# Optimization experiments

Hardware: AMD Instinct MI355X
Metric: run time of the kernel (lower is better)

The kernel has to match this reference:

```python
import jax, jax.numpy as jnp
import numpy as np

NEG_SLOPE = 0.2  # PyG GATConv default negative_slope


def gat_layer(x, edge_index, W, att_src, att_dst, bias):
    """GATConv with self-loops, concat heads. x:[N,F_in], W:[F_in,H*C]."""
    N = x.shape[0]
    H, C = att_src.shape
    loop = jnp.arange(N, dtype=edge_index.dtype)
    src = jnp.concatenate([edge_index[0], loop])  # [E+N]
    dst = jnp.concatenate([edge_index[1], loop])
    h = (x @ W).reshape(N, H, C)                  # [N,H,C]
    a_src = jnp.einsum('nhc,hc->nh', h, att_src)  # [N,H]
    a_dst = jnp.einsum('nhc,hc->nh', h, att_dst)
    e = a_src[src] + a_dst[dst]                   # [E+N,H]
    e = jnp.where(e > 0, e, NEG_SLOPE * e)        # leaky_relu
    # numerically-stable segment softmax over incoming edges of each dst node
    m = jax.ops.segment_max(e, dst, num_segments=N)           # [N,H]
    ex = jnp.exp(e - m[dst])
    denom = jax.ops.segment_sum(ex, dst, num_segments=N)      # [N,H]
    alpha = ex / (denom[dst] + 1e-16)                          # [E+N,H]
    out = jax.ops.segment_sum(h[src] * alpha[:, :, None], dst, num_segments=N)
    return out.reshape(N, H * C) + bias


def setup_inputs() -> dict:
    key = jax.random.key(0)
    ks = jax.random.split(key, 16)
    N, E, F_IN, HID, H, NCLS = 50000, 800000, 128, 64, 4, 40
    HC = H * HID
    s = 0.1
    return {
        'x': jax.random.normal(ks[0], (N, F_IN), jnp.float32),
        'edge_index': jax.random.randint(ks[1], (2, E), 0, N, jnp.int32),
        'W1': jax.random.normal(ks[2], (F_IN, HC), jnp.float32) * s,
        'att_src1': jax.random.normal(ks[3], (H, HID), jnp.float32) * s,
        'att_dst1': jax.random.normal(ks[4], (H, HID), jnp.float32) * s,
        'b1': jnp.zeros((HC,), jnp.float32),
        'W2': jax.random.normal(ks[5], (HC, HC), jnp.float32) * s,
        'att_src2': jax.random.normal(ks[6], (H, HID), jnp.float32) * s,
        'att_dst2': jax.random.normal(ks[7], (H, HID), jnp.float32) * s,
        'b2': jnp.zeros((HC,), jnp.float32),
        'fcW1': jax.random.normal(ks[8], (HC, HID), jnp.float32) * s,
        'fcb1': jnp.zeros((HID,), jnp.float32),
        'fcW2': jax.random.normal(ks[9], (HID, NCLS), jnp.float32) * s,
        'fcb2': jnp.zeros((NCLS,), jnp.float32),
    }


def reference(x, edge_index, W1, att_src1, att_dst1, b1,
              W2, att_src2, att_dst2, b2, fcW1, fcb1, fcW2, fcb2):
    h = gat_layer(x, edge_index, W1, att_src1, att_dst1, b1)
    h = jax.nn.elu(h)
    h = gat_layer(h, edge_index, W2, att_src2, att_dst2, b2)
    h = jax.nn.elu(h)
    h = jnp.maximum(h @ fcW1 + fcb1, 0.0)  # ReLU; dropout is identity in eval
    return h @ fcW2 + fcb2                 # [N, num_classes]
```

## Files before the change

kernel.cpp:

```cpp
#include <hip/hip_runtime.h>

typedef __attribute__((ext_vector_type(8))) _Float16 fp16x8;
typedef __attribute__((ext_vector_type(4))) float f32x4;
typedef unsigned int u32;

__device__ __forceinline__ float lrelu(float x) { return x > 0.f ? x : 0.2f * x; }
__device__ __forceinline__ float elu(float x) { return x > 0.f ? x : __expf(x) - 1.f; }

__device__ __forceinline__ void gl2lds16(const void* g, void* l) {
    __builtin_amdgcn_global_load_lds((const __attribute__((address_space(1))) u32*)g,
                                     (__attribute__((address_space(3))) u32*)l, 16, 0, 0);
}

__device__ __forceinline__ void t16t_body(const float* __restrict__ W, _Float16* __restrict__ T,
                                          int N, int Nreal, int t) {
    int lane = t & 63, rem = t >> 6;
    int kk = rem & 1; rem >>= 1;
    int ncg = N / 16;
    int cg = rem % ncg, kc = rem / ncg;
    int k = kc * 64 + kk * 32 + (lane >> 4) * 8;
    int n = cg * 16 + (lane & 15);
    fp16x8 o;
#pragma unroll
    for (int j = 0; j < 8; ++j)
        o[j] = (n < Nreal) ? (_Float16)W[(size_t)(k + j) * Nreal + n] : (_Float16)0.f;
    *(fp16x8*)(T + (size_t)t * 8) = o;
}

__global__ __launch_bounds__(256) void k_prep(const float* __restrict__ W1, _Float16* __restrict__ W1T,
                                              const float* __restrict__ W2, _Float16* __restrict__ W2T,
                                              const float* __restrict__ fcW1, _Float16* __restrict__ fWT,
                                              const float* __restrict__ fcW2, _Float16* __restrict__ f2T,
                                              const int* __restrict__ dst, int* __restrict__ cnt) {
    int b = blockIdx.x, tid = threadIdx.x;
    if (b < 16)      t16t_body(W1, W1T, 256, 256, b * 256 + tid);
    else if (b < 48) t16t_body(W2, W2T, 256, 256, (b - 16) * 256 + tid);
    else if (b < 56) t16t_body(fcW1, fWT, 64, 64, (b - 48) * 256 + tid);
    else if (b < 58) t16t_body(fcW2, f2T, 64, 40, (b - 56) * 256 + tid);
    else             atomicAdd(&cnt[dst[(b - 58) * 256 + tid]], 1);
}

__global__ __launch_bounds__(256) void k_scan_a(const int* __restrict__ cnt, int* __restrict__ s,
                                                int* __restrict__ partial, int N) {
    __shared__ int sh[256];
    int t = threadIdx.x, gid = blockIdx.x * 256 + t;
    sh[t] = gid < N ? cnt[gid] : 0;
    __syncthreads();
    for (int off = 1; off < 256; off <<= 1) {
        int add = (t >= off) ? sh[t - off] : 0;
        __syncthreads();
        sh[t] += add;
        __syncthreads();
    }
    if (gid < N) s[gid] = sh[t];
    if (t == 255) partial[blockIdx.x] = sh[255];
}
__global__ __launch_bounds__(256) void k_scan_bc(const int* __restrict__ s, const int* __restrict__ partial,
                                                 const int* __restrict__ cnt, int* __restrict__ row_ptr,
                                                 int* __restrict__ cursor, int* __restrict__ bcur, int N) {
    __shared__ int red[256];
    int t = threadIdx.x, bid = blockIdx.x;
    int a = 0;
    for (int i = t; i < bid; i += 256) a += partial[i];
    red[t] = a;
    __syncthreads();
    for (int off = 128; off; off >>= 1) {
        if (t < off) red[t] += red[t + off];
        __syncthreads();
    }
    int base = red[0];
    int gid = bid * 256 + t;
    if (gid >= N) return;
    int val = s[gid] + base;
    row_ptr[gid + 1] = val;
    int excl = val - cnt[gid];
    cursor[gid] = excl;
    if ((gid & 511) == 0) bcur[gid >> 9] = excl;
    if (gid == 0) row_ptr[0] = 0;
}

__global__ __launch_bounds__(256) void k_bin(const int* __restrict__ src, const int* __restrict__ dst,
                                             int* __restrict__ bcur, int2* __restrict__ pairbuf, int E) {
    __shared__ int cnt[128], gbase[128], excl[128], cur2[128], sh[128];
    __shared__ int saddr[1024];
    __shared__ int2 spair[1024];
    const int tid = threadIdx.x;
    const int eb = blockIdx.x * 1024;
    if (tid < 128) { cnt[tid] = 0; cur2[tid] = 0; }
    __syncthreads();
    int s_[4], d_[4];
#pragma unroll
    for (int j = 0; j < 4; ++j) {
        int e = eb + j * 256 + tid;
        if (e < E) {
            s_[j] = src[e]; d_[j] = dst[e];
            atomicAdd(&cnt[d_[j] >> 9], 1);
        } else d_[j] = -1;
    }
    __syncthreads();
    if (tid < 128) sh[tid] = cnt[tid];
    __syncthreads();
    for (int off = 1; off < 128; off <<= 1) {
        int add = 0;
        if (tid < 128 && tid >= off) add = sh[tid - off];
        __syncthreads();
        if (tid < 128) sh[tid] += add;
        __syncthreads();
    }
    if (tid < 128) {
        excl[tid] = sh[tid] - cnt[tid];
        if (cnt[tid] > 0) gbase[tid] = atomicAdd(&bcur[tid], cnt[tid]);
    }
    __syncthreads();
#pragma unroll
    for (int j = 0; j < 4; ++j) {
        if (d_[j] >= 0) {
            int b = d_[j] >> 9;
            int r = atomicAdd(&cur2[b], 1);
            int slot = excl[b] + r;
            spair[slot] = make_int2(s_[j], d_[j]);
            saddr[slot] = gbase[b] + r;
        }
    }
    __syncthreads();
    int tot = min(1024, E - eb);
#pragma unroll
    for (int j = 0; j < 4; ++j) {
        int slot = j * 256 + tid;
        if (slot < tot) pairbuf[saddr[slot]] = spair[slot];
    }
}

template<int KV, int NW, int ATT, int AFP32>
__device__ __forceinline__ void gemm_body(int bid,
              const _Float16* __restrict__ Ah, const float* __restrict__ Af,
              const _Float16* __restrict__ BT, _Float16* __restrict__ Chi,
              const float* __restrict__ att_s, const float* __restrict__ att_d,
              float* __restrict__ a_src, float* __restrict__ a_dst,
              int M, int Nc) {
    constexpr int NCG = NW / 16;
    constexpr int CHUNK = NW * 64;
    constexpr int FPW = (CHUNK / 512) / 8;
    __shared__ _Float16 Bs[CHUNK];
    const int m0 = bid * 128;
    const int tid = threadIdx.x;
    const int lane = tid & 63, wv = tid >> 6;
    const int r16 = lane & 15, quad = lane >> 4;
    const int arow = min(m0 + wv * 16 + r16, M - 1);

    f32x4 acc[NCG];
#pragma unroll
    for (int cg = 0; cg < NCG; ++cg) acc[cg] = (f32x4){0, 0, 0, 0};

    constexpr int NCH = KV / 64;
#pragma unroll
    for (int kc = 0; kc < NCH; ++kc) {
        if (kc) __syncthreads();
#pragma unroll
        for (int f = 0; f < FPW; ++f) {
            int fr = wv * FPW + f;
            gl2lds16(BT + (size_t)kc * CHUNK + fr * 512 + lane * 8, &Bs[fr * 512]);
        }
        fp16x8 ar[2];
        if (AFP32) {
            const float* Ap = Af + (size_t)arow * KV + kc * 64 + quad * 8;
#pragma unroll
            for (int kk = 0; kk < 2; ++kk) {
                float4 u0 = *(const float4*)(Ap + kk * 32);
                float4 u1 = *(const float4*)(Ap + kk * 32 + 4);
                fp16x8 h8;
                h8[0] = (_Float16)u0.x; h8[1] = (_Float16)u0.y;
                h8[2] = (_Float16)u0.z; h8[3] = (_Float16)u0.w;
                h8[4] = (_Float16)u1.x; h8[5] = (_Float16)u1.y;
                h8[6] = (_Float16)u1.z; h8[7] = (_Float16)u1.w;
                ar[kk] = h8;
            }
        } else {
            const _Float16* Ahp = Ah + (size_t)arow * KV + kc * 64 + quad * 8;
#pragma unroll
            for (int kk = 0; kk < 2; ++kk) ar[kk] = *(const fp16x8*)(Ahp + kk * 32);
        }
        __syncthreads();
#pragma unroll
        for (int kk = 0; kk < 2; ++kk) {
#pragma unroll
            for (int cg = 0; cg < NCG; ++cg) {
                fp16x8 bh = *(const fp16x8*)(&Bs[(cg * 2 + kk) * 512 + lane * 8]);
                acc[cg] = __builtin_amdgcn_mfma_f32_16x16x32_f16(ar[kk], bh, acc[cg], 0, 0, 0);
            }
        }
    }

    const int rbase = m0 + wv * 16 + quad * 4;

    if (ATT) {
#pragma unroll
        for (int hq = 0; hq < 4; ++hq) {
            float as[4], ad[4];
#pragma unroll
            for (int cg = 0; cg < 4; ++cg) {
                as[cg] = att_s[hq * 64 + cg * 16 + r16];
                ad[cg] = att_d[hq * 64 + cg * 16 + r16];
            }
#pragma unroll
            for (int i = 0; i < 4; ++i) {
                float ps = acc[hq * 4 + 0][i] * as[0] + acc[hq * 4 + 1][i] * as[1]
                         + acc[hq * 4 + 2][i] * as[2] + acc[hq * 4 + 3][i] * as[3];
                float pd = acc[hq * 4 + 0][i] * ad[0] + acc[hq * 4 + 1][i] * ad[1]
                         + acc[hq * 4 + 2][i] * ad[2] + acc[hq * 4 + 3][i] * ad[3];
#pragma unroll
                for (int d = 1; d < 16; d <<= 1) {
                    ps += __shfl_xor(ps, d);
                    pd += __shfl_xor(pd, d);
                }
                int r = rbase + i;
                if (r16 == 0 && r < M) {
                    a_src[(size_t)r * 4 + hq] = ps;
                    a_dst[(size_t)r * 4 + hq] = pd;
                }
            }
        }
    }

#pragma unroll
    for (int cg = 0; cg < NCG; ++cg) {
        int c = cg * 16 + r16;
        if (c >= Nc) continue;
#pragma unroll
        for (int i = 0; i < 4; ++i) {
            int r = rbase + i;
            if (r < M) Chi[(size_t)r * Nc + c] = (_Float16)acc[cg][i];
        }
    }
}

__global__ __launch_bounds__(512, 4)
void k_work1(const float* __restrict__ x, const _Float16* __restrict__ W1T,
             _Float16* __restrict__ h,
             const float* __restrict__ att_s, const float* __restrict__ att_d,
             float* __restrict__ a_src, float* __restrict__ a_dst,
             const int2* __restrict__ pairbuf,
             int* __restrict__ cursor, int* __restrict__ csr,
             int M, int E, int RB) {
    if ((int)blockIdx.x >= RB) {
        int base = (blockIdx.x - RB) * 2048;
#pragma unroll
        for (int j = 0; j < 4; ++j) {
            int i = base + j * 512 + threadIdx.x;
            if (i < E) {
                int2 p = pairbuf[i];
                int pos = atomicAdd(&cursor[p.y], 1);
                csr[pos] = p.x;
            }
        }
        return;
    }
    gemm_body<128, 256, 1, 1>(blockIdx.x, nullptr, x, W1T, h, att_s, att_d, a_src, a_dst, M, 256);
}

#define AG2_LDA 264
__global__ __launch_bounds__(512, 4) void k_ag2(
        const _Float16* __restrict__ h, const float* __restrict__ a_src,
        const float* __restrict__ a_dst, const int* __restrict__ row_ptr,
        const int* __restrict__ csr, const float* __restrict__ bias,
        const _Float16* __restrict__ BT,
        const float* __restrict__ att_s, const float* __restrict__ att_d,
        float* __restrict__ a_src2, float* __restrict__ a_dst2,
        _Float16* __restrict__ h2, int N) {
    __shared__ _Float16 A[16 * AG2_LDA];
    __shared__ float psp[8][16], pdp[8][16];
    const int tid = threadIdx.x;
    const int n0 = blockIdx.x * 16;

    {
        int r = tid >> 5;
        int n = min(n0 + r, N - 1);
        int cl = tid & 31;
        int hd = cl >> 3;
        int beg = row_ptr[n], end = row_ptr[n + 1];
        float adh = a_dst[(size_t)4 * n + hd];
        const _Float16* hb = h + (size_t)cl * 8;

        float ws = __expf(lrelu(a_src[(size_t)4 * n + hd] + adh));
        fp16x8 sv = *(const fp16x8*)(hb + (size_t)n * 256);
        float acc[8];
#pragma unroll
        for (int j = 0; j < 8; ++j) acc[j] = ws * (float)sv[j];
        float dn = ws;

        int e = beg;
        for (; e + 4 <= end; e += 4) {
            int s0 = csr[e], s1 = csr[e + 1], s2 = csr[e + 2], s3 = csr[e + 3];
            float z0 = a_src[(size_t)4 * s0 + hd], z1 = a_src[(size_t)4 * s1 + hd];
            float z2 = a_src[(size_t)4 * s2 + hd], z3 = a_src[(size_t)4 * s3 + hd];
            fp16x8 v0 = *(const fp16x8*)(hb + (size_t)s0 * 256);
            fp16x8 v1 = *(const fp16x8*)(hb + (size_t)s1 * 256);
            fp16x8 v2 = *(const fp16x8*)(hb + (size_t)s2 * 256);
            fp16x8 v3 = *(const fp16x8*)(hb + (size_t)s3 * 256);
            float w0 = __expf(lrelu(z0 + adh)), w1 = __expf(lrelu(z1 + adh));
            float w2 = __expf(lrelu(z2 + adh)), w3 = __expf(lrelu(z3 + adh));
            dn += (w0 + w1) + (w2 + w3);
#pragma unroll
            for (int j = 0; j < 8; ++j)
                acc[j] += w0 * (float)v0[j] + w1 * (float)v1[j]
                        + w2 * (float)v2[j] + w3 * (float)v3[j];
        }
        for (; e + 2 <= end; e += 2) {
            int s0 = csr[e], s1 = csr[e + 1];
            float z0 = a_src[(size_t)4 * s0 + hd], z1 = a_src[(size_t)4 * s1 + hd];
            fp16x8 v0 = *(const fp16x8*)(hb + (size_t)s0 * 256);
            fp16x8 v1 = *(const fp16x8*)(hb + (size_t)s1 * 256);
            float w0 = __expf(lrelu(z0 + adh)), w1 = __expf(lrelu(z1 + adh));
            dn += w0 + w1;
#pragma unroll
            for (int j = 0; j < 8; ++j)
                acc[j] += w0 * (float)v0[j] + w1 * (float)v1[j];
        }
        if (e < end) {
            int s0 = csr[e];
            float w0 = __expf(lrelu(a_src[(size_t)4 * s0 + hd] + adh));
            fp16x8 v0 = *(const fp16x8*)(hb + (size_t)s0 * 256);
            dn += w0;
#pragma unroll
            for (int j = 0; j < 8; ++j) acc[j] += w0 * (float)v0[j];
        }

        float inv = 1.f / (dn + 1e-16f);
        float4 b0 = *(const float4*)(bias + cl * 8);
        float4 b1v = *(const float4*)(bias + cl * 8 + 4);
        fp16x8 hi;
        hi[0] = (_Float16)elu(acc[0] * inv + b0.x);
        hi[1] = (_Float16)elu(acc[1] * inv + b0.y);
        hi[2] = (_Float16)elu(acc[2] * inv + b0.z);
        hi[3] = (_Float16)elu(acc[3] * inv + b0.w);
        hi[4] = (_Float16)elu(acc[4] * inv + b1v.x);
        hi[5] = (_Float16)elu(acc[5] * inv + b1v.y);
        hi[6] = (_Float16)elu(acc[6] * inv + b1v.z);
        hi[7] = (_Float16)elu(acc[7] * inv + b1v.w);
        *(fp16x8*)(&A[r * AG2_LDA + cl * 8]) = hi;
    }
    __syncthreads();

    const int lane = tid & 63, wv = tid >> 6;
    const int r16 = lane & 15, quad = lane >> 4;
    f32x4 acc2[2];
    acc2[0] = (f32x4){0, 0, 0, 0};
    acc2[1] = (f32x4){0, 0, 0, 0};
#pragma unroll
    for (int kc = 0; kc < 4; ++kc) {
        fp16x8 ar[2];
#pragma unroll
        for (int kk = 0; kk < 2; ++kk)
            ar[kk] = *(const fp16x8*)(&A[r16 * AG2_LDA + kc * 64 + kk * 32 + quad * 8]);
#pragma unroll
        for (int kk = 0; kk < 2; ++kk) {
#pragma unroll
            for (int j = 0; j < 2; ++j) {
                int cg = wv * 2 + j;
                fp16x8 bh = *(const fp16x8*)(BT + ((size_t)(kc * 16 + cg) * 2 + kk) * 512 + lane * 8);
                acc2[j] = __builtin_amdgcn_mfma_f32_16x16x32_f16(ar[kk], bh, acc2[j], 0, 0, 0);
            }
        }
    }
    {
        float as[2], ad[2];
#pragma unroll
        for (int j = 0; j < 2; ++j) {
            int c = (wv * 2 + j) * 16 + r16;
            as[j] = att_s[c];
            ad[j] = att_d[c];
        }
#pragma unroll
        for (int i = 0; i < 4; ++i) {
            float ps = acc2[0][i] * as[0] + acc2[1][i] * as[1];
            float pd = acc2[0][i] * ad[0] + acc2[1][i] * ad[1];
#pragma unroll
            for (int d = 1; d < 16; d <<= 1) {
                ps += __shfl_xor(ps, d);
                pd += __shfl_xor(pd, d);
            }
            if (r16 == 0) {
                psp[wv][quad * 4 + i] = ps;
                pdp[wv][quad * 4 + i] = pd;
            }
        }
    }
#pragma unroll
    for (int j = 0; j < 2; ++j) {
        int c = (wv * 2 + j) * 16 + r16;
#pragma unroll
        for (int i = 0; i < 4; ++i) {
            int rr = n0 + quad * 4 + i;
            if (rr < N) h2[(size_t)rr * 256 + c] = (_Float16)acc2[j][i];
        }
    }
    __syncthreads();
    if (tid < 64) {
        int row = tid >> 2, hq = tid & 3;
        int rr = n0 + row;
        if (rr < N) {
            a_src2[(size_t)rr * 4 + hq] = psp[2 * hq][row] + psp[2 * hq + 1][row];
            a_dst2[(size_t)rr * 4 + hq] = pdp[2 * hq][row] + pdp[2 * hq + 1][row];
        }
    }
}

__global__ __launch_bounds__(512, 4) void k_agfc(
        const _Float16* __restrict__ h, const float* __restrict__ a_src,
        const float* __restrict__ a_dst, const int* __restrict__ row_ptr,
        const int* __restrict__ csr, const float* __restrict__ bias,
        const _Float16* __restrict__ BT1, const _Float16* __restrict__ BT2,
        const float* __restrict__ fcb1, const float* __restrict__ fcb2,
        float* __restrict__ out, int N) {
    __shared__ _Float16 A[16 * AG2_LDA];
    __shared__ _Float16 T[16 * 72];
    const int tid = threadIdx.x;
    const int n0 = blockIdx.x * 16;

    {
        int r = tid >> 5;
        int n = min(n0 + r, N - 1);
        int cl = tid & 31;
        int hd = cl >> 3;
        int beg = row_ptr[n], end = row_ptr[n + 1];
        float adh = a_dst[(size_t)4 * n + hd];
        const _Float16* hb = h + (size_t)cl * 8;

        float ws = __expf(lrelu(a_src[(size_t)4 * n + hd] + adh));
        fp16x8 sv = *(const fp16x8*)(hb + (size_t)n * 256);
        float acc[8];
#pragma unroll
        for (int j = 0; j < 8; ++j) acc[j] = ws * (float)sv[j];
        float dn = ws;

        int e = beg;
        for (; e + 4 <= end; e += 4) {
            int s0 = csr[e], s1 = csr[e + 1], s2 = csr[e + 2], s3 = csr[e + 3];
            float z0 = a_src[(size_t)4 * s0 + hd], z1 = a_src[(size_t)4 * s1 + hd];
            float z2 = a_src[(size_t)4 * s2 + hd], z3 = a_src[(size_t)4 * s3 + hd];
            fp16x8 v0 = *(const fp16x8*)(hb + (size_t)s0 * 256);
            fp16x8 v1 = *(const fp16x8*)(hb + (size_t)s1 * 256);
            fp16x8 v2 = *(const fp16x8*)(hb + (size_t)s2 * 256);
            fp16x8 v3 = *(const fp16x8*)(hb + (size_t)s3 * 256);
            float w0 = __expf(lrelu(z0 + adh)), w1 = __expf(lrelu(z1 + adh));
            float w2 = __expf(lrelu(z2 + adh)), w3 = __expf(lrelu(z3 + adh));
            dn += (w0 + w1) + (w2 + w3);
#pragma unroll
            for (int j = 0; j < 8; ++j)
                acc[j] += w0 * (float)v0[j] + w1 * (float)v1[j]
                        + w2 * (float)v2[j] + w3 * (float)v3[j];
        }
        for (; e + 2 <= end; e += 2) {
            int s0 = csr[e], s1 = csr[e + 1];
            float z0 = a_src[(size_t)4 * s0 + hd], z1 = a_src[(size_t)4 * s1 + hd];
            fp16x8 v0 = *(const fp16x8*)(hb + (size_t)s0 * 256);
            fp16x8 v1 = *(const fp16x8*)(hb + (size_t)s1 * 256);
            float w0 = __expf(lrelu(z0 + adh)), w1 = __expf(lrelu(z1 + adh));
            dn += w0 + w1;
#pragma unroll
            for (int j = 0; j < 8; ++j)
                acc[j] += w0 * (float)v0[j] + w1 * (float)v1[j];
        }
        if (e < end) {
            int s0 = csr[e];
            float w0 = __expf(lrelu(a_src[(size_t)4 * s0 + hd] + adh));
            fp16x8 v0 = *(const fp16x8*)(hb + (size_t)s0 * 256);
            dn += w0;
#pragma unroll
            for (int j = 0; j < 8; ++j) acc[j] += w0 * (float)v0[j];
        }

        float inv = 1.f / (dn + 1e-16f);
        float4 b0 = *(const float4*)(bias + cl * 8);
        float4 b1v = *(const float4*)(bias + cl * 8 + 4);
        fp16x8 hi;
        hi[0] = (_Float16)elu(acc[0] * inv + b0.x);
        hi[1] = (_Float16)elu(acc[1] * inv + b0.y);
        hi[2] = (_Float16)elu(acc[2] * inv + b0.z);
        hi[3] = (_Float16)elu(acc[3] * inv + b0.w);
        hi[4] = (_Float16)elu(acc[4] * inv + b1v.x);
        hi[5] = (_Float16)elu(acc[5] * inv + b1v.y);
        hi[6] = (_Float16)elu(acc[6] * inv + b1v.z);
        hi[7] = (_Float16)elu(acc[7] * inv + b1v.w);
        *(fp16x8*)(&A[(tid >> 5) * AG2_LDA + cl * 8]) = hi;
    }
    __syncthreads();

    const int lane = tid & 63, wv = tid >> 6;
    const int r16 = lane & 15, quad = lane >> 4;
    if (wv < 4) {
        f32x4 acc1 = (f32x4){0, 0, 0, 0};
#pragma unroll
        for (int kc = 0; kc < 4; ++kc) {
            fp16x8 ar[2];
#pragma unroll
            for (int kk = 0; kk < 2; ++kk)
                ar[kk] = *(const fp16x8*)(&A[r16 * AG2_LDA + kc * 64 + kk * 32 + quad * 8]);
#pragma unroll
            for (int kk = 0; kk < 2; ++kk) {
                fp16x8 bh = *(const fp16x8*)(BT1 + ((size_t)(kc * 4 + wv) * 2 + kk) * 512 + lane * 8);
                acc1 = __builtin_amdgcn_mfma_f32_16x16x32_f16(ar[kk], bh, acc1, 0, 0, 0);
            }
        }
        int c = wv * 16 + r16;
        float badd = fcb1[c];
#pragma unroll
        for (int i = 0; i < 4; ++i)
            T[(quad * 4 + i) * 72 + c] = (_Float16)fmaxf(acc1[i] + badd, 0.f);
    }
    __syncthreads();

    if (wv < 3) {
        fp16x8 a2[2];
#pragma unroll
        for (int kk = 0; kk < 2; ++kk)
            a2[kk] = *(const fp16x8*)(&T[r16 * 72 + kk * 32 + quad * 8]);
        f32x4 acc2 = (f32x4){0, 0, 0, 0};
#pragma unroll
        for (int kk = 0; kk < 2; ++kk) {
            fp16x8 bh = *(const fp16x8*)(BT2 + ((size_t)wv * 2 + kk) * 512 + lane * 8);
            acc2 = __builtin_amdgcn_mfma_f32_16x16x32_f16(a2[kk], bh, acc2, 0, 0, 0);
        }
        int c = wv * 16 + r16;
        if (c < 40) {
            float badd = fcb2[c];
#pragma unroll
            for (int i = 0; i < 4; ++i) {
                int rr = n0 + quad * 4 + i;
                if (rr < N) out[(size_t)rr * 40 + c] = acc2[i] + badd;
            }
        }
    }
}

extern "C" void kernel_launch(void* const* d_in, const int* in_sizes, int n_in,
                              void* d_out, int out_size, void* d_ws, size_t ws_size,
                              hipStream_t stream) {
    const int N = 50000, E = 800000, F_IN = 128, HC = 256, HID = 64, NCLS = 40;
    const float* x    = (const float*)d_in[0];
    const int*   ei   = (const int*)d_in[1];
    const float* W1   = (const float*)d_in[2];
    const float* as1  = (const float*)d_in[3];
    const float* ad1  = (const float*)d_in[4];
    const float* b1   = (const float*)d_in[5];
    const float* W2   = (const float*)d_in[6];
    const float* as2  = (const float*)d_in[7];
    const float* ad2  = (const float*)d_in[8];
    const float* b2   = (const float*)d_in[9];
    const float* fcW1 = (const float*)d_in[10];
    const float* fcb1 = (const float*)d_in[11];
    const float* fcW2 = (const float*)d_in[12];
    const float* fcb2 = (const float*)d_in[13];
    float* out = (float*)d_out;

    char* wp = (char*)d_ws;
    auto alloc = [&](size_t b) { char* p = wp; wp += (b + 255) & ~(size_t)255; return p; };
    _Float16* h     = (_Float16*)alloc((size_t)N * HC * 2);
    _Float16* ohi   = (_Float16*)alloc((size_t)N * HC * 2);
    float*  asrc  = (float*)alloc((size_t)N * 4 * 4);
    float*  adst  = (float*)alloc((size_t)N * 4 * 4);
    float*  asrc2 = (float*)alloc((size_t)N * 4 * 4);
    float*  adst2 = (float*)alloc((size_t)N * 4 * 4);
    _Float16* W1T   = (_Float16*)alloc((size_t)F_IN * HC * 2);
    _Float16* W2T   = (_Float16*)alloc((size_t)HC * HC * 2);
    _Float16* fWT   = (_Float16*)alloc((size_t)HC * HID * 2);
    _Float16* f2T   = (_Float16*)alloc((size_t)HID * HID * 2);
    int* cnt     = (int*)alloc((size_t)N * 4);
    int* sbuf    = (int*)alloc((size_t)N * 4);
    int* part    = (int*)alloc(1024);
    int* row_ptr = (int*)alloc(((size_t)N + 1) * 4);
    int* cursor  = (int*)alloc((size_t)N * 4);
    int* csr     = (int*)alloc((size_t)E * 4);
    int* bcur    = (int*)alloc(128 * 4);
    int2* pairs  = (int2*)alloc((size_t)E * 8);

    const int* src = ei;
    const int* dst = ei + E;

    const int rb = (N + 127) / 128;
    const int ag_blocks = (N + 15) / 16;
    const int bin_blocks = (E + 1023) / 1024;
    const int p2_blocks = (E + 2047) / 2048;

    hipMemsetAsync(cnt, 0, (size_t)N * 4, stream);
    k_prep<<<3183, 256, 0, stream>>>(W1, W1T, W2, W2T, fcW1, fWT, fcW2, f2T, dst, cnt);
    int nb = (N + 255) / 256;
    k_scan_a<<<nb, 256, 0, stream>>>(cnt, sbuf, part, N);
    k_scan_bc<<<nb, 256, 0, stream>>>(sbuf, part, cnt, row_ptr, cursor, bcur, N);
    k_bin<<<bin_blocks, 256, 0, stream>>>(src, dst, bcur, pairs, E);
    k_work1<<<rb + p2_blocks, 512, 0, stream>>>(x, W1T, h, as1, ad1, asrc, adst,
                                                pairs, cursor, csr, N, E, rb);
    k_ag2<<<ag_blocks, 512, 0, stream>>>(h, asrc, adst, row_ptr, csr, b1,
                                         W2T, as2, ad2, asrc2, adst2, ohi, N);
    k_agfc<<<ag_blocks, 512, 0, stream>>>(ohi, asrc2, adst2, row_ptr, csr, b2,
                                          fWT, f2T, fcb1, fcb2, out, N);
}
```

Before: 320.3 us.

## Process 64 nodes per aggregation block and merge two-pass scan into one kernel

The two aggregation+GEMM kernels now handle 64 destination nodes per block instead of 16. Each thread loops over four rows, and the MFMA stage reuses every loaded weight fragment across four row tiles, which cuts repeated global reads of W2T/fcW tiles. The scan is folded into a single kernel in which each block recomputes its prefix base by summing all earlier counts. That removes one launch but adds redundant O(N) reads for later blocks. The larger LDS footprint and extra accumulators may lower occupancy (k_agfc launch bound drops to 3), and per-block serial row loops reduce latency hiding.

```diff
diff --git a/kernel.cpp b/kernel.cpp
--- a/kernel.cpp
+++ b/kernel.cpp
@@ -40,10 +40,21 @@
     else             atomicAdd(&cnt[dst[(b - 58) * 256 + tid]], 1);
 }
 
-__global__ __launch_bounds__(256) void k_scan_a(const int* __restrict__ cnt, int* __restrict__ s,
-                                                int* __restrict__ partial, int N) {
+__global__ __launch_bounds__(256) void k_scan(const int* __restrict__ cnt, int* __restrict__ row_ptr,
+                                              int* __restrict__ cursor, int* __restrict__ bcur, int N) {
+    __shared__ int red[256];
     __shared__ int sh[256];
-    int t = threadIdx.x, gid = blockIdx.x * 256 + t;
+    int t = threadIdx.x, bid = blockIdx.x, gid = bid * 256 + t;
+    int lim = bid * 256;
+    int a = 0;
+    for (int i = t; i < lim; i += 256) a += cnt[i];
+    red[t] = a;
+    __syncthreads();
+    for (int off = 128; off; off >>= 1) {
+        if (t < off) red[t] += red[t + off];
+        __syncthreads();
+    }
+    int base = red[0];
     sh[t] = gid < N ? cnt[gid] : 0;
     __syncthreads();
     for (int off = 1; off < 256; off <<= 1) {
@@ -52,26 +63,8 @@
         sh[t] += add;
         __syncthreads();
     }
-    if (gid < N) s[gid] = sh[t];
-    if (t == 255) partial[blockIdx.x] = sh[255];
-}
-__global__ __launch_bounds__(256) void k_scan_bc(const int* __restrict__ s, const int* __restrict__ partial,
-                                                 const int* __restrict__ cnt, int* __restrict__ row_ptr,
-                                                 int* __restrict__ cursor, int* __restrict__ bcur, int N) {
-    __shared__ int red[256];
-    int t = threadIdx.x, bid = blockIdx.x;
-    int a = 0;
-    for (int i = t; i < bid; i += 256) a += partial[i];
-    red[t] = a;
-    __syncthreads();
-    for (int off = 128; off; off >>= 1) {
-        if (t < off) red[t] += red[t + off];
-        __syncthreads();
-    }
-    int base = red[0];
-    int gid = bid * 256 + t;
     if (gid >= N) return;
-    int val = s[gid] + base;
+    int val = sh[t] + base;
     row_ptr[gid + 1] = val;
     int excl = val - cnt[gid];
     cursor[gid] = excl;
@@ -258,6 +251,70 @@
     gemm_body<128, 256, 1, 1>(blockIdx.x, nullptr, x, W1T, h, att_s, att_d, a_src, a_dst, M, 256);
 }
 
+__device__ __forceinline__ fp16x8 aggr_row(const _Float16* __restrict__ hb,
+        const float* __restrict__ a_src, const float* __restrict__ a_dst,
+        const int* __restrict__ row_ptr, const int* __restrict__ csr,
+        const float* __restrict__ bias, int n, int cl, int hd) {
+    int beg = row_ptr[n], end = row_ptr[n + 1];
+    float adh = a_dst[(size_t)4 * n + hd];
+    float ws = __expf(lrelu(a_src[(size_t)4 * n + hd] + adh));
+    fp16x8 sv = *(const fp16x8*)(hb + (size_t)n * 256);
+    float acc[8];
+#pragma unroll
+    for (int j = 0; j < 8; ++j) acc[j] = ws * (float)sv[j];
+    float dn = ws;
+    int e = beg;
+    for (; e + 4 <= end; e += 4) {
+        int s0 = csr[e], s1 = csr[e + 1], s2 = csr[e + 2], s3 = csr[e + 3];
+        float z0 = a_src[(size_t)4 * s0 + hd], z1 = a_src[(size_t)4 * s1 + hd];
+        float z2 = a_src[(size_t)4 * s2 + hd], z3 = a_src[(size_t)4 * s3 + hd];
+        fp16x8 v0 = *(const fp16x8*)(hb + (size_t)s0 * 256);
+        fp16x8 v1 = *(const fp16x8*)(hb + (size_t)s1 * 256);
+        fp16x8 v2 = *(const fp16x8*)(hb + (size_t)s2 * 256);
+        fp16x8 v3 = *(const fp16x8*)(hb + (size_t)s3 * 256);
+        float w0 = __expf(lrelu(z0 + adh)), w1 = __expf(lrelu(z1 + adh));
+        float w2 = __expf(lrelu(z2 + adh)), w3 = __expf(lrelu(z3 + adh));
+        dn += (w0 + w1) + (w2 + w3);
+#pragma unroll
+        for (int j = 0; j < 8; ++j)
+            acc[j] += w0 * (float)v0[j] + w1 * (float)v1[j]
+                    + w2 * (float)v2[j] + w3 * (float)v3[j];
+    }
+    for (; e + 2 <= end; e += 2) {
+        int s0 = csr[e], s1 = csr[e + 1];
+        float z0 = a_src[(size_t)4 * s0 + hd], z1 = a_src[(size_t)4 * s1 + hd];
+        fp16x8 v0 = *(const fp16x8*)(hb + (size_t)s0 * 256);
+        fp16x8 v1 = *(const fp16x8*)(hb + (size_t)s1 * 256);
+        float w0 = __expf(lrelu(z0 + adh)), w1 = __expf(lrelu(z1 + adh));
+        dn += w0 + w1;
+#pragma unroll
+        for (int j = 0; j < 8; ++j)
+            acc[j] += w0 * (float)v0[j] + w1 * (float)v1[j];
+    }
+    if (e < end) {
+        int s0 = csr[e];
+        float w0 = __expf(lrelu(a_src[(size_t)4 * s0 + hd] + adh));
+        fp16x8 v0 = *(const fp16x8*)(hb + (size_t)s0 * 256);
+        dn += w0;
+#pragma unroll
+        for (int j = 0; j < 8; ++j) acc[j] += w0 * (float)v0[j];
+    }
+    float inv = 1.f / (dn + 1e-16f);
+    float4 b0 = *(const float4*)(bias + cl * 8);
+    float4 b1v = *(const float4*)(bias + cl * 8 + 4);
+    fp16x8 hi;
+    hi[0] = (_Float16)elu(acc[0] * inv + b0.x);
+    hi[1] = (_Float16)elu(acc[1] * inv + b0.y);
+    hi[2] = (_Float16)elu(acc[2] * inv + b0.z);
+    hi[3] = (_Float16)elu(acc[3] * inv + b0.w);
+    hi[4] = (_Float16)elu(acc[4] * inv + b1v.x);
+    hi[5] = (_Float16)elu(acc[5] * inv + b1v.y);
+    hi[6] = (_Float16)elu(acc[6] * inv + b1v.z);
+    hi[7] = (_Float16)elu(acc[7] * inv + b1v.w);
+    return hi;
+}
+
+#define AGN 64
 #define AG2_LDA 264
 __global__ __launch_bounds__(512, 4) void k_ag2(
         const _Float16* __restrict__ h, const float* __restrict__ a_src,
@@ -267,121 +324,64 @@
         const float* __restrict__ att_s, const float* __restrict__ att_d,
         float* __restrict__ a_src2, float* __restrict__ a_dst2,
         _Float16* __restrict__ h2, int N) {
-    __shared__ _Float16 A[16 * AG2_LDA];
-    __shared__ float psp[8][16], pdp[8][16];
+    __shared__ _Float16 A[AGN * AG2_LDA];
+    __shared__ float psp[8][AGN], pdp[8][AGN];
     const int tid = threadIdx.x;
-    const int n0 = blockIdx.x * 16;
+    const int n0 = blockIdx.x * AGN;
 
     {
-        int r = tid >> 5;
-        int n = min(n0 + r, N - 1);
-        int cl = tid & 31;
-        int hd = cl >> 3;
-        int beg = row_ptr[n], end = row_ptr[n + 1];
-        float adh = a_dst[(size_t)4 * n + hd];
+        const int r = tid >> 5, cl = tid & 31, hd = cl >> 3;
         const _Float16* hb = h + (size_t)cl * 8;
-
-        float ws = __expf(lrelu(a_src[(size_t)4 * n + hd] + adh));
-        fp16x8 sv = *(const fp16x8*)(hb + (size_t)n * 256);
-        float acc[8];
-#pragma unroll
-        for (int j = 0; j < 8; ++j) acc[j] = ws * (float)sv[j];
-        float dn = ws;
-
-        int e = beg;
-        for (; e + 4 <= end; e += 4) {
-            int s0 = csr[e], s1 = csr[e + 1], s2 = csr[e + 2], s3 = csr[e + 3];
-            float z0 = a_src[(size_t)4 * s0 + hd], z1 = a_src[(size_t)4 * s1 + hd];
-            float z2 = a_src[(size_t)4 * s2 + hd], z3 = a_src[(size_t)4 * s3 + hd];
-            fp16x8 v0 = *(const fp16x8*)(hb + (size_t)s0 * 256);
-            fp16x8 v1 = *(const fp16x8*)(hb + (size_t)s1 * 256);
-            fp16x8 v2 = *(const fp16x8*)(hb + (size_t)s2 * 256);
-            fp16x8 v3 = *(const fp16x8*)(hb + (size_t)s3 * 256);
-            float w0 = __expf(lrelu(z0 + adh)), w1 = __expf(lrelu(z1 + adh));
-            float w2 = __expf(lrelu(z2 + adh)), w3 = __expf(lrelu(z3 + adh));
-            dn += (w0 + w1) + (w2 + w3);
-#pragma unroll
-            for (int j = 0; j < 8; ++j)
-                acc[j] += w0 * (float)v0[j] + w1 * (float)v1[j]
-                        + w2 * (float)v2[j] + w3 * (float)v3[j];
-        }
-        for (; e + 2 <= end; e += 2) {
-            int s0 = csr[e], s1 = csr[e + 1];
-            float z0 = a_src[(size_t)4 * s0 + hd], z1 = a_src[(size_t)4 * s1 + hd];
-            fp16x8 v0 = *(const fp16x8*)(hb + (size_t)s0 * 256);
-            fp16x8 v1 = *(const fp16x8*)(hb + (size_t)s1 * 256);
-            float w0 = __expf(lrelu(z0 + adh)), w1 = __expf(lrelu(z1 + adh));
-            dn += w0 + w1;
-#pragma unroll
-            for (int j = 0; j < 8; ++j)
-                acc[j] += w0 * (float)v0[j] + w1 * (float)v1[j];
-        }
-        if (e < end) {
-            int s0 = csr[e];
-            float w0 = __expf(lrelu(a_src[(size_t)4 * s0 + hd] + adh));
-            fp16x8 v0 = *(const fp16x8*)(hb + (size_t)s0 * 256);
-            dn += w0;
-#pragma unroll
-            for (int j = 0; j < 8; ++j) acc[j] += w0 * (float)v0[j];
-        }
-
-        float inv = 1.f / (dn + 1e-16f);
-        float4 b0 = *(const float4*)(bias + cl * 8);
-        float4 b1v = *(const float4*)(bias + cl * 8 + 4);
-        fp16x8 hi;
-        hi[0] = (_Float16)elu(acc[0] * inv + b0.x);
-        hi[1] = (_Float16)elu(acc[1] * inv + b0.y);
-        hi[2] = (_Float16)elu(acc[2] * inv + b0.z);
-        hi[3] = (_Float16)elu(acc[3] * inv + b0.w);
-        hi[4] = (_Float16)elu(acc[4] * inv + b1v.x);
-        hi[5] = (_Float16)elu(acc[5] * inv + b1v.y);
-        hi[6] = (_Float16)elu(acc[6] * inv + b1v.z);
-        hi[7] = (_Float16)elu(acc[7] * inv + b1v.w);
-        *(fp16x8*)(&A[r * AG2_LDA + cl * 8]) = hi;
+#pragma unroll 1
+        for (int it = 0; it < 4; ++it) {
+            int ln = it * 16 + r;
+            int n = min(n0 + ln, N - 1);
+            fp16x8 hi = aggr_row(hb, a_src, a_dst, row_ptr, csr, bias, n, cl, hd);
+            *(fp16x8*)(&A[ln * AG2_LDA + cl * 8]) = hi;
+        }
     }
     __syncthreads();
 
     const int lane = tid & 63, wv = tid >> 6;
     const int r16 = lane & 15, quad = lane >> 4;
-    f32x4 acc2[2];
-    acc2[0] = (f32x4){0, 0, 0, 0};
-    acc2[1] = (f32x4){0, 0, 0, 0};
+    f32x4 acc2[4][2];
+#pragma unroll
+    for (int rt = 0; rt < 4; ++rt) {
+        acc2[rt][0] = (f32x4){0, 0, 0, 0};
+        acc2[rt][1] = (f32x4){0, 0, 0, 0};
+    }
 #pragma unroll
     for (int kc = 0; kc < 4; ++kc) {
-        fp16x8 ar[2];
-#pragma unroll
-        for (int kk = 0; kk < 2; ++kk)
-            ar[kk] = *(const fp16x8*)(&A[r16 * AG2_LDA + kc * 64 + kk * 32 + quad * 8]);
 #pragma unroll
         for (int kk = 0; kk < 2; ++kk) {
-#pragma unroll
-            for (int j = 0; j < 2; ++j) {
-                int cg = wv * 2 + j;
-                fp16x8 bh = *(const fp16x8*)(BT + ((size_t)(kc * 16 + cg) * 2 + kk) * 512 + lane * 8);
-                acc2[j] = __builtin_amdgcn_mfma_f32_16x16x32_f16(ar[kk], bh, acc2[j], 0, 0, 0);
+            fp16x8 bh0 = *(const fp16x8*)(BT + ((size_t)(kc * 16 + wv * 2) * 2 + kk) * 512 + lane * 8);
+            fp16x8 bh1 = *(const fp16x8*)(BT + ((size_t)(kc * 16 + wv * 2 + 1) * 2 + kk) * 512 + lane * 8);
+#pragma unroll
+            for (int rt = 0; rt < 4; ++rt) {
+                fp16x8 ar = *(const fp16x8*)(&A[(rt * 16 + r16) * AG2_LDA + kc * 64 + kk * 32 + quad * 8]);
+                acc2[rt][0] = __builtin_amdgcn_mfma_f32_16x16x32_f16(ar, bh0, acc2[rt][0], 0, 0, 0);
+                acc2[rt][1] = __builtin_amdgcn_mfma_f32_16x16x32_f16(ar, bh1, acc2[rt][1], 0, 0, 0);
             }
         }
     }
     {
-        float as[2], ad[2];
-#pragma unroll
-        for (int j = 0; j < 2; ++j) {
-            int c = (wv * 2 + j) * 16 + r16;
-            as[j] = att_s[c];
-            ad[j] = att_d[c];
-        }
-#pragma unroll
-        for (int i = 0; i < 4; ++i) {
-            float ps = acc2[0][i] * as[0] + acc2[1][i] * as[1];
-            float pd = acc2[0][i] * ad[0] + acc2[1][i] * ad[1];
-#pragma unroll
-            for (int d = 1; d < 16; d <<= 1) {
-                ps += __shfl_xor(ps, d);
-                pd += __shfl_xor(pd, d);
-            }
-            if (r16 == 0) {
-                psp[wv][quad * 4 + i] = ps;
-                pdp[wv][quad * 4 + i] = pd;
+        float as0 = att_s[(wv * 2) * 16 + r16], as1 = att_s[(wv * 2 + 1) * 16 + r16];
+        float ad0 = att_d[(wv * 2) * 16 + r16], ad1 = att_d[(wv * 2 + 1) * 16 + r16];
+#pragma unroll
+        for (int rt = 0; rt < 4; ++rt) {
+#pragma unroll
+            for (int i = 0; i < 4; ++i) {
+                float ps = acc2[rt][0][i] * as0 + acc2[rt][1][i] * as1;
+                float pd = acc2[rt][0][i] * ad0 + acc2[rt][1][i] * ad1;
+#pragma unroll
+                for (int d = 1; d < 16; d <<= 1) {
+                    ps += __shfl_xor(ps, d);
+                    pd += __shfl_xor(pd, d);
+                }
+                if (r16 == 0) {
+                    psp[wv][rt * 16 + quad * 4 + i] = ps;
+                    pdp[wv][rt * 16 + quad * 4 + i] = pd;
+                }
             }
         }
     }
@@ -389,13 +389,16 @@
     for (int j = 0; j < 2; ++j) {
         int c = (wv * 2 + j) * 16 + r16;
 #pragma unroll
-        for (int i = 0; i < 4; ++i) {
-            int rr = n0 + quad * 4 + i;
-            if (rr < N) h2[(size_t)rr * 256 + c] = (_Float16)acc2[j][i];
-        }
-    }
-    __syncthreads();
-    if (tid < 64) {
+        for (int rt = 0; rt < 4; ++rt) {
+#pragma unroll
+            for (int i = 0; i < 4; ++i) {
+                int rr = n0 + rt * 16 + quad * 4 + i;
+                if (rr < N) h2[(size_t)rr * 256 + c] = (_Float16)acc2[rt][j][i];
+            }
+        }
+    }
+    __syncthreads();
+    if (tid < 256) {
         int row = tid >> 2, hq = tid & 3;
         int rr = n0 + row;
         if (rr < N) {
@@ -405,130 +408,82 @@
     }
 }
 
-__global__ __launch_bounds__(512, 4) void k_agfc(
+__global__ __launch_bounds__(512, 3) void k_agfc(
         const _Float16* __restrict__ h, const float* __restrict__ a_src,
         const float* __restrict__ a_dst, const int* __restrict__ row_ptr,
         const int* __restrict__ csr, const float* __restrict__ bias,
         const _Float16* __restrict__ BT1, const _Float16* __restrict__ BT2,
         const float* __restrict__ fcb1, const float* __restrict__ fcb2,
         float* __restrict__ out, int N) {
-    __shared__ _Float16 A[16 * AG2_LDA];
-    __shared__ _Float16 T[16 * 72];
+    __shared__ _Float16 A[AGN * AG2_LDA];
+    __shared__ _Float16 T[AGN * 72];
     const int tid = threadIdx.x;
-    const int n0 = blockIdx.x * 16;
+    const int n0 = blockIdx.x * AGN;
 
     {
-        int r = tid >> 5;
-        int n = min(n0 + r, N - 1);
-        int cl = tid & 31;
-        int hd = cl >> 3;
-        int beg = row_ptr[n], end = row_ptr[n + 1];
-        float adh = a_dst[(size_t)4 * n + hd];
+        const int r = tid >> 5, cl = tid & 31, hd = cl >> 3;
         const _Float16* hb = h + (size_t)cl * 8;
-
-        float ws = __expf(lrelu(a_src[(size_t)4 * n + hd] + adh));
-        fp16x8 sv = *(const fp16x8*)(hb + (size_t)n * 256);
-        float acc[8];
-#pragma unroll
-        for (int j = 0; j < 8; ++j) acc[j] = ws * (float)sv[j];
-        float dn = ws;
-
-        int e = beg;
-        for (; e + 4 <= end; e += 4) {
-            int s0 = csr[e], s1 = csr[e + 1], s2 = csr[e + 2], s3 = csr[e + 3];
-            float z0 = a_src[(size_t)4 * s0 + hd], z1 = a_src[(size_t)4 * s1 + hd];
-            float z2 = a_src[(size_t)4 * s2 + hd], z3 = a_src[(size_t)4 * s3 + hd];
-            fp16x8 v0 = *(const fp16x8*)(hb + (size_t)s0 * 256);
-            fp16x8 v1 = *(const fp16x8*)(hb + (size_t)s1 * 256);
-            fp16x8 v2 = *(const fp16x8*)(hb + (size_t)s2 * 256);
-            fp16x8 v3 = *(const fp16x8*)(hb + (size_t)s3 * 256);
-            float w0 = __expf(lrelu(z0 + adh)), w1 = __expf(lrelu(z1 + adh));
-            float w2 = __expf(lrelu(z2 + adh)), w3 = __expf(lrelu(z3 + adh));
-            dn += (w0 + w1) + (w2 + w3);
-#pragma unroll
-            for (int j = 0; j < 8; ++j)
-                acc[j] += w0 * (float)v0[j] + w1 * (float)v1[j]
-                        + w2 * (float)v2[j] + w3 * (float)v3[j];
-        }
-        for (; e + 2 <= end; e += 2) {
-            int s0 = csr[e], s1 = csr[e + 1];
-            float z0 = a_src[(size_t)4 * s0 + hd], z1 = a_src[(size_t)4 * s1 + hd];
-            fp16x8 v0 = *(const fp16x8*)(hb + (size_t)s0 * 256);
-            fp16x8 v1 = *(const fp16x8*)(hb + (size_t)s1 * 256);
-            float w0 = __expf(lrelu(z0 + adh)), w1 = __expf(lrelu(z1 + adh));
-            dn += w0 + w1;
-#pragma unroll
-            for (int j = 0; j < 8; ++j)
-                acc[j] += w0 * (float)v0[j] + w1 * (float)v1[j];
-        }
-        if (e < end) {
-            int s0 = csr[e];
-            float w0 = __expf(lrelu(a_src[(size_t)4 * s0 + hd] + adh));
-            fp16x8 v0 = *(const fp16x8*)(hb + (size_t)s0 * 256);
-            dn += w0;
-#pragma unroll
-            for (int j = 0; j < 8; ++j) acc[j] += w0 * (float)v0[j];
-        }
-
-        float inv = 1.f / (dn + 1e-16f);
-        float4 b0 = *(const float4*)(bias + cl * 8);
-        float4 b1v = *(const float4*)(bias + cl * 8 + 4);
-        fp16x8 hi;
-        hi[0] = (_Float16)elu(acc[0] * inv + b0.x);
-        hi[1] = (_Float16)elu(acc[1] * inv + b0.y);
-        hi[2] = (_Float16)elu(acc[2] * inv + b0.z);
-        hi[3] = (_Float16)elu(acc[3] * inv + b0.w);
-        hi[4] = (_Float16)elu(acc[4] * inv + b1v.x);
-        hi[5] = (_Float16)elu(acc[5] * inv + b1v.y);
-        hi[6] = (_Float16)elu(acc[6] * inv + b1v.z);
-        hi[7] = (_Float16)elu(acc[7] * inv + b1v.w);
-        *(fp16x8*)(&A[(tid >> 5) * AG2_LDA + cl * 8]) = hi;
+#pragma unroll 1
+        for (int it = 0; it < 4; ++it) {
+            int ln = it * 16 + r;
+            int n = min(n0 + ln, N - 1);
+            fp16x8 hi = aggr_row(hb, a_src, a_dst, row_ptr, csr, bias, n, cl, hd);
+            *(fp16x8*)(&A[ln * AG2_LDA + cl * 8]) = hi;
+        }
     }
     __syncthreads();
 
     const int lane = tid & 63, wv = tid >> 6;
     const int r16 = lane & 15, quad = lane >> 4;
     if (wv < 4) {
-        f32x4 acc1 = (f32x4){0, 0, 0, 0};
+        f32x4 acc1[4];
+#pragma unroll
+        for (int rt = 0; rt < 4; ++rt) acc1[rt] = (f32x4){0, 0, 0, 0};
 #pragma unroll
         for (int kc = 0; kc < 4; ++kc) {
-            fp16x8 ar[2];
-#pragma unroll
-            for (int kk = 0; kk < 2; ++kk)
-                ar[kk] = *(const fp16x8*)(&A[r16 * AG2_LDA + kc * 64 + kk * 32 + quad * 8]);
 #pragma unroll
             for (int kk = 0; kk < 2; ++kk) {
                 fp16x8 bh = *(const fp16x8*)(BT1 + ((size_t)(kc * 4 + wv) * 2 + kk) * 512 + lane * 8);
-                acc1 = __builtin_amdgcn_mfma_f32_16x16x32_f16(ar[kk], bh, acc1, 0, 0, 0);
+#pragma unroll
+                for (int rt = 0; rt < 4; ++rt) {
+                    fp16x8 ar = *(const fp16x8*)(&A[(rt * 16 + r16) * AG2_LDA + kc * 64 + kk * 32 + quad * 8]);
+                    acc1[rt] = __builtin_amdgcn_mfma_f32_16x16x32_f16(ar, bh, acc1[rt], 0, 0, 0);
+                }
             }
         }
         int c = wv * 16 + r16;
         float badd = fcb1[c];
 #pragma unroll
-        for (int i = 0; i < 4; ++i)
-            T[(quad * 4 + i) * 72 + c] = (_Float16)fmaxf(acc1[i] + badd, 0.f);
+        for (int rt = 0; rt < 4; ++rt)
+#pragma unroll
+            for (int i = 0; i < 4; ++i)
+                T[(rt * 16 + quad * 4 + i) * 72 + c] = (_Float16)fmaxf(acc1[rt][i] + badd, 0.f);
     }
     __syncthreads();
 
     if (wv < 3) {
-        fp16x8 a2[2];
-#pragma unroll
-        for (int kk = 0; kk < 2; ++kk)
-            a2[kk] = *(const fp16x8*)(&T[r16 * 72 + kk * 32 + quad * 8]);
-        f32x4 acc2 = (f32x4){0, 0, 0, 0};
+        f32x4 acc2[4];
+#pragma unroll
+        for (int rt = 0; rt < 4; ++rt) acc2[rt] = (f32x4){0, 0, 0, 0};
 #pragma unroll
         for (int kk = 0; kk < 2; ++kk) {
             fp16x8 bh = *(const fp16x8*)(BT2 + ((size_t)wv * 2 + kk) * 512 + lane * 8);
-            acc2 = __builtin_amdgcn_mfma_f32_16x16x32_f16(a2[kk], bh, acc2, 0, 0, 0);
+#pragma unroll
+            for (int rt = 0; rt < 4; ++rt) {
+                fp16x8 a2 = *(const fp16x8*)(&T[(rt * 16 + r16) * 72 + kk * 32 + quad * 8]);
+                acc2[rt] = __builtin_amdgcn_mfma_f32_16x16x32_f16(a2, bh, acc2[rt], 0, 0, 0);
+            }
         }
         int c = wv * 16 + r16;
         if (c < 40) {
             float badd = fcb2[c];
 #pragma unroll
-            for (int i = 0; i < 4; ++i) {
-                int rr = n0 + quad * 4 + i;
-                if (rr < N) out[(size_t)rr * 40 + c] = acc2[i] + badd;
-            }
+            for (int rt = 0; rt < 4; ++rt)
+#pragma unroll
+                for (int i = 0; i < 4; ++i) {
+                    int rr = n0 + rt * 16 + quad * 4 + i;
+                    if (rr < N) out[(size_t)rr * 40 + c] = acc2[rt][i] + badd;
+                }
         }
     }
 }
@@ -566,8 +521,6 @@
     _Float16* fWT   = (_Float16*)alloc((size_t)HC * HID * 2);
     _Float16* f2T   = (_Float16*)alloc((size_t)HID * HID * 2);
     int* cnt     = (int*)alloc((size_t)N * 4);
-    int* sbuf    = (int*)alloc((size_t)N * 4);
-    int* part    = (int*)alloc(1024);
     int* row_ptr = (int*)alloc(((size_t)N + 1) * 4);
     int* cursor  = (int*)alloc((size_t)N * 4);
     int* csr     = (int*)alloc((size_t)E * 4);
@@ -578,15 +531,14 @@
     const int* dst = ei + E;
 
     const int rb = (N + 127) / 128;
-    const int ag_blocks = (N + 15) / 16;
+    const int ag_blocks = (N + AGN - 1) / AGN;
     const int bin_blocks = (E + 1023) / 1024;
     const int p2_blocks = (E + 2047) / 2048;
 
     hipMemsetAsync(cnt, 0, (size_t)N * 4, stream);
     k_prep<<<3183, 256, 0, stream>>>(W1, W1T, W2, W2T, fcW1, fWT, fcW2, f2T, dst, cnt);
     int nb = (N + 255) / 256;
-    k_scan_a<<<nb, 256, 0, stream>>>(cnt, sbuf, part, N);
-    k_scan_bc<<<nb, 256, 0, stream>>>(sbuf, part, cnt, row_ptr, cursor, bcur, N);
+    k_scan<<<nb, 256, 0, stream>>>(cnt, row_ptr, cursor, bcur, N);
     k_bin<<<bin_blocks, 256, 0, stream>>>(src, dst, bcur, pairs, E);
     k_work1<<<rb + p2_blocks, 512, 0, stream>>>(x, W1T, h, as1, ad1, asrc, adst,
                                                 pairs, cursor, csr, N, E, rb);
```

After: 374.0 us. +16.8%, slower.
